# Kernel optimization log

Measured on AMD Instinct MI355X. Metric: run time of the kernel, lower is better.

## Reference

```python
import jax, jax.numpy as jnp
import numpy as np

EPS = 1e-5  # F.instance_norm default eps


def _inorm(x, axis):
    # instance norm (no affine), biased variance, over `axis`
    m = jnp.mean(x, axis=axis, keepdims=True)
    v = jnp.mean((x - m) ** 2, axis=axis, keepdims=True)
    return (x - m) * jax.lax.rsqrt(v + EPS)


def setup_inputs() -> dict:
    key = jax.random.key(0)
    ks = jax.random.split(key, 8)
    C, N, H, W = 256, 8192, 96, 96
    wscale = C ** -0.5  # keep logits in a sane range
    q = jax.random.normal(ks[0], (N, C), jnp.float32)
    k = jax.random.normal(ks[1], (1, C, H, W), jnp.float32)
    qw = jax.random.normal(ks[2], (C, C), jnp.float32) * wscale
    qb = jax.random.normal(ks[3], (C,), jnp.float32) * 0.1
    kw = jax.random.normal(ks[4], (C, C), jnp.float32) * wscale
    kb = jax.random.normal(ks[5], (C,), jnp.float32) * 0.1
    sw = jax.random.normal(ks[6], (C, C), jnp.float32) * wscale
    sb = jax.random.normal(ks[7], (C,), jnp.float32) * 0.1
    return {"q": q, "k": k, "qw": qw, "qb": qb, "kw": kw, "kb": kb, "sw": sw, "sb": sb}


def reference(q, k, qw, qb, kw, kb, sw, sb):
    # q: (N, C) content features; k: (1, C, H, W) style features
    C = q.shape[1]
    qc = q.T                       # (C, N)  == q.T.unsqueeze(0) without batch dim
    st = k[0].reshape(C, -1)       # (C, HW) style values (flattened)

    qn = _inorm(qc, 1)             # instance norm over N per channel
    qe = (qw @ qn + qb[:, None]).T # Conv1d 1x1 -> (N, C)

    kn = _inorm(st, 1)             # instance norm over H*W per channel
    ke = kw @ kn + kb[:, None]     # Conv2d 1x1 -> (C, HW)

    se = (sw @ st + sb[:, None]).T # Conv2d 1x1 -> (HW, C)

    scale = C ** -0.5
    attn = jax.nn.softmax((qe @ ke) * scale, axis=-1)   # (N, HW)

    mean = attn @ se                                    # (N, C)
    var = jax.nn.relu(attn @ (se * se) - mean * mean)   # (N, C)
    std = jnp.sqrt(var)

    cs = qn.T * std + mean          # instance_norm(c) * std + mean, (N, C)
    return cs
```

## Files before the change

kernel.cpp:

```cpp
#include <hip/hip_runtime.h>

typedef __attribute__((ext_vector_type(8))) short short8;
typedef __attribute__((ext_vector_type(4))) float float4v;

#define CDIM 256
#define NQ   8192
#define HWN  9216

static __device__ __forceinline__ unsigned short f2bf(float f) {
  union { float f; unsigned int i; } v; v.f = f;
  unsigned int r = v.i + 0x7FFFu + ((v.i >> 16) & 1u);
  return (unsigned short)(r >> 16);
}

__global__ __launch_bounds__(256) void stats_all_kernel(const float* __restrict__ q, const float* __restrict__ k0,
                                                        float* __restrict__ pq, float* __restrict__ pq2,
                                                        float* __restrict__ mk, float* __restrict__ rk,
                                                        float* __restrict__ sdk) {
  int b = blockIdx.x, t = threadIdx.x;
  if (b < 256) {
    const float4* q4 = (const float4*)(q + (size_t)b * 32 * CDIM);
    float sx = 0, sy = 0, sz = 0, sw = 0, tx = 0, ty = 0, tz = 0, tw = 0;
    for (int i = t; i < 32 * 64; i += 256) {
      float4 v = q4[i];
      sx += v.x; sy += v.y; sz += v.z; sw += v.w;
      tx += v.x * v.x; ty += v.y * v.y; tz += v.z * v.z; tw += v.w * v.w;
    }
    __shared__ float4 sA[256], sB[256];
    sA[t] = make_float4(sx, sy, sz, sw); sB[t] = make_float4(tx, ty, tz, tw);
    __syncthreads();
    if (t < 64) {
      float4 a = sA[t], b2 = sB[t];
      #pragma unroll
      for (int r = 1; r < 4; r++) {
        float4 u = sA[t + r * 64], w2 = sB[t + r * 64];
        a.x += u.x; a.y += u.y; a.z += u.z; a.w += u.w;
        b2.x += w2.x; b2.y += w2.y; b2.z += w2.z; b2.w += w2.w;
      }
      ((float4*)pq)[b * 64 + t] = a;
      ((float4*)pq2)[b * 64 + t] = b2;
    }
  } else {
    __shared__ float rs[256], rs2[256];
    int c = b - 256;
    float s = 0.f, s2 = 0.f;
    const float4* row = (const float4*)(k0 + (size_t)c * HWN);
    for (int j = t; j < HWN / 4; j += 256) {
      float4 v = row[j];
      s += v.x + v.y + v.z + v.w;
      s2 += v.x * v.x + v.y * v.y + v.z * v.z + v.w * v.w;
    }
    rs[t] = s; rs2[t] = s2; __syncthreads();
    for (int off = 128; off > 0; off >>= 1) {
      if (t < off) { rs[t] += rs[t + off]; rs2[t] += rs2[t + off]; }
      __syncthreads();
    }
    if (t == 0) {
      float mean = rs[0] / (float)HWN;
      float var = fmaxf(rs2[0] / (float)HWN - mean * mean, 0.f);
      mk[c] = mean; rk[c] = rsqrtf(var + 1e-5f); sdk[c] = sqrtf(var + 1e-5f);
    }
  }
}

__global__ __launch_bounds__(256) void cvtall_kernel(const float* __restrict__ qw, const float* __restrict__ kw,
                                                     const float* __restrict__ sw, const float* __restrict__ sb,
                                                     unsigned short* __restrict__ qwb, unsigned short* __restrict__ kwb,
                                                     unsigned short* __restrict__ swb2,
                                                     const float* __restrict__ sdk, const float* __restrict__ mk,
                                                     const float* __restrict__ pq, const float* __restrict__ pq2,
                                                     float* __restrict__ mq, float* __restrict__ rq,
                                                     float* __restrict__ bias2) {
  int b = blockIdx.x, t = threadIdx.x;
  if (b < 128) {
    const float* src = b < 64 ? qw : kw;
    unsigned short* dst = b < 64 ? qwb : kwb;
    int i = (b & 63) * 256 + t;
    float4 v = ((const float4*)src)[i];
    union { unsigned short o[4]; uint2 u; } w;
    w.o[0] = f2bf(v.x); w.o[1] = f2bf(v.y); w.o[2] = f2bf(v.z); w.o[3] = f2bf(v.w);
    ((uint2*)dst)[i] = w.u;
  } else if (b < 192) {
    int i = (b - 128) * 256 + t;
    int c0 = (i * 4) & 255;
    float4 v = ((const float4*)sw)[i];
    union { unsigned short o[4]; uint2 u; } w;
    w.o[0] = f2bf(v.x * sdk[c0 + 0]); w.o[1] = f2bf(v.y * sdk[c0 + 1]);
    w.o[2] = f2bf(v.z * sdk[c0 + 2]); w.o[3] = f2bf(v.w * sdk[c0 + 3]);
    ((uint2*)swb2)[i] = w.u;
  } else if (b == 192) {
    int c = t;
    float s = 0, s2 = 0;
    for (int bb = 0; bb < 256; bb++) { s += pq[bb * 256 + c]; s2 += pq2[bb * 256 + c]; }
    float mean = s / (float)NQ;
    float var = s2 / (float)NQ - mean * mean;
    mq[c] = mean; rq[c] = rsqrtf(fmaxf(var, 0.f) + 1e-5f);
  } else {
    int r = t;
    float acc = 0.f;
    for (int k = 0; k < 256; k++) acc += sw[r * 256 + k] * mk[k];
    bias2[r] = acc + sb[r];
  }
}

__global__ __launch_bounds__(256) void ktrans_kernel(const float* __restrict__ k0,
                                                     const float* __restrict__ mk, const float* __restrict__ rk,
                                                     unsigned short* __restrict__ stn) {
  __shared__ float tile[32][33];
  int p0 = blockIdx.x * 32, c0 = blockIdx.y * 32;
  int t = threadIdx.x;
  int pl = t & 31, cl = t >> 5;
  #pragma unroll
  for (int r = 0; r < 4; r++) {
    int c = cl + r * 8;
    tile[c][pl] = k0[(size_t)(c0 + c) * HWN + p0 + pl];
  }
  __syncthreads();
  int cl2 = t & 31, pl2 = t >> 5;
  float mean = mk[c0 + cl2], rinv = rk[c0 + cl2];
  #pragma unroll
  for (int r = 0; r < 4; r++) {
    int p = pl2 + r * 8;
    float f = tile[cl2][p];
    stn[(size_t)(p0 + p) * CDIM + c0 + cl2] = f2bf((f - mean) * rinv);
  }
}

__global__ __launch_bounds__(256) void gemms_kernel(const float* __restrict__ qf,
                                                    const float* __restrict__ mq, const float* __restrict__ rq,
                                                    const unsigned short* __restrict__ qwb, const float* __restrict__ qb,
                                                    unsigned short* __restrict__ Qs,
                                                    const unsigned short* __restrict__ stn,
                                                    const unsigned short* __restrict__ kwb, const float* __restrict__ kb,
                                                    unsigned short* __restrict__ Km,
                                                    const unsigned short* __restrict__ swb2, const float* __restrict__ bias2,
                                                    unsigned short* __restrict__ VseT, unsigned short* __restrict__ Vse2T) {
  int b = blockIdx.x, t = threadIdx.x;
  int w = t >> 6, lane = t & 63, g = lane >> 4, li = lane & 15;
  float4v acc[16];
  #pragma unroll
  for (int i = 0; i < 16; i++) acc[i] = (float4v){0.f, 0.f, 0.f, 0.f};

  if (b < 128) {
    int m0 = b * 64;
    const float* abase = qf + (size_t)(m0 + w * 16 + li) * CDIM + g * 8;
    #pragma unroll
    for (int kc = 0; kc < 8; kc++) {
      int c0 = kc * 32 + g * 8;
      float4 f0 = *(const float4*)(abase + kc * 32);
      float4 f1 = *(const float4*)(abase + kc * 32 + 4);
      float4 m0v = *(const float4*)(mq + c0), m1v = *(const float4*)(mq + c0 + 4);
      float4 r0v = *(const float4*)(rq + c0), r1v = *(const float4*)(rq + c0 + 4);
      union { unsigned short o[8]; short8 s; } a;
      a.o[0] = f2bf((f0.x - m0v.x) * r0v.x); a.o[1] = f2bf((f0.y - m0v.y) * r0v.y);
      a.o[2] = f2bf((f0.z - m0v.z) * r0v.z); a.o[3] = f2bf((f0.w - m0v.w) * r0v.w);
      a.o[4] = f2bf((f1.x - m1v.x) * r1v.x); a.o[5] = f2bf((f1.y - m1v.y) * r1v.y);
      a.o[6] = f2bf((f1.z - m1v.z) * r1v.z); a.o[7] = f2bf((f1.w - m1v.w) * r1v.w);
      #pragma unroll
      for (int ct = 0; ct < 16; ct++) {
        short8 bb = *(const short8*)(qwb + (size_t)(ct * 16 + li) * CDIM + kc * 32 + g * 8);
        acc[ct] = __builtin_amdgcn_mfma_f32_16x16x32_bf16(a.s, bb, acc[ct], 0, 0, 0);
      }
    }
    #pragma unroll
    for (int ct = 0; ct < 16; ct++) {
      int col = ct * 16 + li;
      #pragma unroll
      for (int j = 0; j < 4; j++) {
        int row = m0 + w * 16 + g * 4 + j;
        float v = (acc[ct][j] + qb[col]) * (0.0625f * 1.4426950408889634f);
        Qs[(size_t)row * CDIM + col] = f2bf(v);
      }
    }
  } else if (b < 272) {
    int m0 = (b - 128) * 64;
    const unsigned short* abase = stn + (size_t)(m0 + w * 16 + li) * CDIM + g * 8;
    #pragma unroll
    for (int kc = 0; kc < 8; kc++) {
      short8 a = *(const short8*)(abase + kc * 32);
      #pragma unroll
      for (int ct = 0; ct < 16; ct++) {
        short8 bb = *(const short8*)(kwb + (size_t)(ct * 16 + li) * CDIM + kc * 32 + g * 8);
        acc[ct] = __builtin_amdgcn_mfma_f32_16x16x32_bf16(a, bb, acc[ct], 0, 0, 0);
      }
    }
    #pragma unroll
    for (int ct = 0; ct < 16; ct++) {
      int col = ct * 16 + li;
      #pragma unroll
      for (int j = 0; j < 4; j++) {
        int row = m0 + w * 16 + g * 4 + j;
        Km[(size_t)row * CDIM + col] = f2bf(acc[ct][j] + kb[col]);
      }
    }
  } else {
    int bb2 = b - 272;
    int m0 = (bb2 & 3) * 64, n0 = (bb2 >> 2) * 256;
    const unsigned short* abase = swb2 + (size_t)(m0 + w * 16 + li) * CDIM + g * 8;
    #pragma unroll
    for (int kc = 0; kc < 8; kc++) {
      short8 a = *(const short8*)(abase + kc * 32);
      #pragma unroll
      for (int ct = 0; ct < 16; ct++) {
        short8 bb = *(const short8*)(stn + (size_t)(n0 + ct * 16 + li) * CDIM + kc * 32 + g * 8);
        acc[ct] = __builtin_amdgcn_mfma_f32_16x16x32_bf16(a, bb, acc[ct], 0, 0, 0);
      }
    }
    #pragma unroll
    for (int ct = 0; ct < 16; ct++) {
      int col = n0 + ct * 16 + li;
      #pragma unroll
      for (int j = 0; j < 4; j++) {
        int row = m0 + w * 16 + g * 4 + j;
        float v = acc[ct][j] + bias2[row];
        VseT[(size_t)row * HWN + col] = f2bf(v);
        Vse2T[(size_t)row * HWN + col] = f2bf(v * v);
      }
    }
  }
}

static __device__ __forceinline__ void issue_K(int p0, int w, int lane,
                                               const unsigned short* __restrict__ Km,
                                               unsigned short* K_buf) {
  #pragma unroll
  for (int j2 = 0; j2 < 2; j2++) {
    int i16 = (j2 * 8 + w) * 64 + lane;
    int row = i16 >> 5;
    int chc = (i16 & 31) ^ (row & 15);
    const unsigned short* src = Km + (size_t)(p0 + row) * CDIM + chc * 8;
    unsigned short* dst = K_buf + (j2 * 8 + w) * 512;
    __builtin_amdgcn_global_load_lds((const __attribute__((address_space(1))) unsigned int*)src,
                                     (__attribute__((address_space(3))) unsigned int*)dst, 16, 0, 0);
  }
}

static __device__ __forceinline__ void issue_V(int p0, int w, int lane,
                                               const unsigned short* __restrict__ VseT,
                                               const unsigned short* __restrict__ Vse2T,
                                               unsigned short* V_buf) {
  #pragma unroll
  for (int j2 = 0; j2 < 4; j2++) {
    int i16 = (j2 * 8 + w) * 64 + lane;
    int vd = i16 >> 2;
    int gc = (i16 & 3) ^ ((vd ^ (vd >> 2)) & 3);
    const unsigned short* src = (vd < 256 ? VseT + (size_t)vd * HWN
                                          : Vse2T + (size_t)(vd - 256) * HWN) + p0 + gc * 8;
    unsigned short* dst = V_buf + (j2 * 8 + w) * 512;
    __builtin_amdgcn_global_load_lds((const __attribute__((address_space(1))) unsigned int*)src,
                                     (__attribute__((address_space(3))) unsigned int*)dst, 16, 0, 0);
  }
}

__global__ __launch_bounds__(512, 1) void attn_kernel(const unsigned short* __restrict__ Qs,
                                                      const unsigned short* __restrict__ Km,
                                                      const unsigned short* __restrict__ VseT,
                                                      const unsigned short* __restrict__ Vse2T,
                                                      float* __restrict__ Op, float2* __restrict__ ml,
                                                      int tiles_per_g, int G) {
  __shared__ __align__(16) unsigned short K_lds[2][32 * 256];
  __shared__ __align__(16) unsigned short V_lds[2][512 * 32];
  __shared__ __align__(16) unsigned short P_scr[8 * 640];

  const int t = threadIdx.x;
  const int w = t >> 6, lane = t & 63;
  const int g4 = lane >> 4, li = lane & 15;

  int bid = blockIdx.x, qb, g;
  if (G == 4) { g = (bid & 7) >> 1; qb = ((bid & 1) << 5) + (bid >> 3); }
  else        { g = bid % G;        qb = bid / G; }
  const int n0 = qb * 128;
  const int p_begin = g * tiles_per_g * 32;

  short8 qf[8];
  {
    const unsigned short* qbase = Qs + (size_t)(n0 + w * 16 + li) * CDIM + g4 * 8;
    #pragma unroll
    for (int kc = 0; kc < 8; kc++) qf[kc] = *(const short8*)(qbase + kc * 32);
  }
  float4v O[32];
  #pragma unroll
  for (int i = 0; i < 32; i++) O[i] = (float4v){0.f, 0.f, 0.f, 0.f};
  float4v s_acc = (float4v){0.f, 0.f, 0.f, 0.f};
  float m[4] = {-1e30f, -1e30f, -1e30f, -1e30f};
  const short8 ones = (short8){0x3F80, 0x3F80, 0x3F80, 0x3F80, 0x3F80, 0x3F80, 0x3F80, 0x3F80};

  issue_K(p_begin, w, lane, Km, K_lds[0]);
  issue_V(p_begin, w, lane, VseT, Vse2T, V_lds[0]);

  for (int it = 0; it < tiles_per_g; ++it) {
    asm volatile("s_waitcnt vmcnt(0)" ::: "memory");
    __builtin_amdgcn_s_barrier();
    asm volatile("" ::: "memory");
    if (it + 1 < tiles_per_g) {
      issue_K(p_begin + (it + 1) * 32, w, lane, Km, K_lds[(it + 1) & 1]);
      issue_V(p_begin + (it + 1) * 32, w, lane, VseT, Vse2T, V_lds[(it + 1) & 1]);
    }

    const unsigned short* Kc = K_lds[it & 1];
    float4v S0 = (float4v){0.f, 0.f, 0.f, 0.f}, S1 = (float4v){0.f, 0.f, 0.f, 0.f};
    __builtin_amdgcn_s_setprio(1);
    #pragma unroll
    for (int kc = 0; kc < 8; kc++) {
      int c = kc * 4 + g4;
      short8 b0 = *(const short8*)((const char*)Kc + li * 512 + ((c ^ li) << 4));
      short8 b1 = *(const short8*)((const char*)Kc + (16 + li) * 512 + ((c ^ li) << 4));
      S0 = __builtin_amdgcn_mfma_f32_16x16x32_bf16(qf[kc], b0, S0, 0, 0, 0);
      S1 = __builtin_amdgcn_mfma_f32_16x16x32_bf16(qf[kc], b1, S1, 0, 0, 0);
    }
    __builtin_amdgcn_s_setprio(0);

    float pmax[4], corr[4];
    #pragma unroll
    for (int j = 0; j < 4; j++) {
      float mx = fmaxf(S0[j], S1[j]);
      #pragma unroll
      for (int msk = 1; msk < 16; msk <<= 1) mx = fmaxf(mx, __shfl_xor(mx, msk, 64));
      pmax[j] = mx;
    }
    int needs = ((pmax[0] > m[0] + 5.f) || (pmax[1] > m[1] + 5.f) ||
                 (pmax[2] > m[2] + 5.f) || (pmax[3] > m[3] + 5.f)) ? 1 : 0;
    if (needs) {
      #pragma unroll
      for (int j = 0; j < 4; j++) {
        float mn = fmaxf(m[j], pmax[j]);
        corr[j] = exp2f(m[j] - mn);
        m[j] = mn;
      }
    }
    unsigned short* Pw = P_scr + w * 640;
    #pragma unroll
    for (int j = 0; j < 4; j++) {
      float e0 = exp2f(S0[j] - m[j]);
      float e1 = exp2f(S1[j] - m[j]);
      int row = g4 * 4 + j;
      Pw[row * 40 + li] = f2bf(e0);
      Pw[row * 40 + 16 + li] = f2bf(e1);
    }
    if (__any(needs)) {
      #pragma unroll
      for (int j = 0; j < 4; j++) s_acc[j] *= corr[j];
      #pragma unroll
      for (int i = 0; i < 32; i++) {
        O[i][0] *= corr[0]; O[i][1] *= corr[1]; O[i][2] *= corr[2]; O[i][3] *= corr[3];
      }
    }

    short8 pa = *(const short8*)(Pw + li * 40 + g4 * 8);
    const unsigned short* Vc = V_lds[it & 1];
    __builtin_amdgcn_s_setprio(1);
    s_acc = __builtin_amdgcn_mfma_f32_16x16x32_bf16(pa, ones, s_acc, 0, 0, 0);
    #pragma unroll
    for (int vt = 0; vt < 32; vt++) {
      int vd = vt * 16 + li;
      int kc2 = g4 ^ ((vd ^ (vd >> 2)) & 3);
      short8 vb = *(const short8*)((const char*)Vc + vd * 64 + (kc2 << 4));
      O[vt] = __builtin_amdgcn_mfma_f32_16x16x32_bf16(pa, vb, O[vt], 0, 0, 0);
    }
    __builtin_amdgcn_s_setprio(0);
  }

  #pragma unroll
  for (int vt = 0; vt < 32; vt++) {
    #pragma unroll
    for (int j = 0; j < 4; j++) {
      int n = n0 + w * 16 + g4 * 4 + j;
      int vd = vt * 16 + li;
      Op[((size_t)g * NQ + n) * 512 + vd] = O[vt][j];
    }
  }
  if (li == 0) {
    #pragma unroll
    for (int j = 0; j < 4; j++) {
      int n = n0 + w * 16 + g4 * 4 + j;
      ml[(size_t)g * NQ + n] = make_float2(m[j], s_acc[j]);
    }
  }
}

__global__ __launch_bounds__(256) void combine_kernel(const float* __restrict__ Op, const float2* __restrict__ ml,
                                                      const float* __restrict__ q,
                                                      const float* __restrict__ mq, const float* __restrict__ rq,
                                                      float* __restrict__ out, int G) {
  int t = threadIdx.x;
  int rl = t >> 6, j = t & 63;
  int n = blockIdx.x * 4 + rl, c0 = j * 4;
  __shared__ float wsm[4][8];
  if (j == 0) {
    float mstar = -1e30f;
    float mg[8], lg[8];
    for (int g = 0; g < G; g++) {
      float2 v = ml[(size_t)g * NQ + n];
      mg[g] = v.x; lg[g] = v.y;
      mstar = fmaxf(mstar, v.x);
    }
    float L = 0.f;
    for (int g = 0; g < G; g++) L += lg[g] * exp2f(mg[g] - mstar);
    float Li = 1.f / L;
    for (int g = 0; g < G; g++) wsm[rl][g] = exp2f(mg[g] - mstar) * Li;
  }
  __syncthreads();
  float4 of = make_float4(0, 0, 0, 0), o2 = make_float4(0, 0, 0, 0);
  for (int g = 0; g < G; g++) {
    size_t base = ((size_t)g * NQ + n) * 512;
    float wg = wsm[rl][g];
    float4 a = *(const float4*)(Op + base + c0);
    float4 b = *(const float4*)(Op + base + 256 + c0);
    of.x += wg * a.x; of.y += wg * a.y; of.z += wg * a.z; of.w += wg * a.w;
    o2.x += wg * b.x; o2.y += wg * b.y; o2.z += wg * b.z; o2.w += wg * b.w;
  }
  float4 qv = *(const float4*)(q + (size_t)n * CDIM + c0);
  float4 mv = *(const float4*)(mq + c0);
  float4 rv = *(const float4*)(rq + c0);
  float4 ov;
  ov.x = (qv.x - mv.x) * rv.x * sqrtf(fmaxf(o2.x - of.x * of.x, 0.f)) + of.x;
  ov.y = (qv.y - mv.y) * rv.y * sqrtf(fmaxf(o2.y - of.y * of.y, 0.f)) + of.y;
  ov.z = (qv.z - mv.z) * rv.z * sqrtf(fmaxf(o2.z - of.z * of.z, 0.f)) + of.z;
  ov.w = (qv.w - mv.w) * rv.w * sqrtf(fmaxf(o2.w - of.w * of.w, 0.f)) + of.w;
  *(float4*)(out + (size_t)n * CDIM + c0) = ov;
}

extern "C" void kernel_launch(void* const* d_in, const int* in_sizes, int n_in,
                              void* d_out, int out_size, void* d_ws, size_t ws_size,
                              hipStream_t stream) {
  const float* q  = (const float*)d_in[0];
  const float* k0 = (const float*)d_in[1];
  const float* qw = (const float*)d_in[2];
  const float* qb = (const float*)d_in[3];
  const float* kw = (const float*)d_in[4];
  const float* kb = (const float*)d_in[5];
  const float* sw = (const float*)d_in[6];
  const float* sb = (const float*)d_in[7];
  float* out = (float*)d_out;

  char* ws = (char*)d_ws;
  float* mq   = (float*)ws; ws += 1024;
  float* rq   = (float*)ws; ws += 1024;
  float* mk   = (float*)ws; ws += 1024;
  float* rk   = (float*)ws; ws += 1024;
  float* sdk  = (float*)ws; ws += 1024;
  float* bias2= (float*)ws; ws += 1024;
  float* pq   = (float*)ws; ws += 256 * 256 * 4;
  float* pq2  = (float*)ws; ws += 256 * 256 * 4;
  unsigned short* qwb  = (unsigned short*)ws; ws += 65536 * 2;
  unsigned short* kwb  = (unsigned short*)ws; ws += 65536 * 2;
  unsigned short* swb2 = (unsigned short*)ws; ws += 65536 * 2;
  unsigned short* Qs    = (unsigned short*)ws; ws += (size_t)NQ * CDIM * 2;
  unsigned short* stn   = (unsigned short*)ws; ws += (size_t)HWN * CDIM * 2;
  unsigned short* Km    = (unsigned short*)ws; ws += (size_t)HWN * CDIM * 2;
  unsigned short* VseT  = (unsigned short*)ws; ws += (size_t)HWN * CDIM * 2;
  unsigned short* Vse2T = (unsigned short*)ws; ws += (size_t)HWN * CDIM * 2;

  size_t base_used = (size_t)(ws - (char*)d_ws);
  int G = 4;
  const int gcand[3] = {4, 2, 1};
  for (int i = 0; i < 3; i++) {
    G = gcand[i];
    size_t need = base_used + (size_t)G * ((size_t)NQ * 512 * 4 + (size_t)NQ * 8);
    if (need <= ws_size) break;
  }
  float*  Opart = (float*)ws;                 ws += (size_t)G * NQ * 512 * 4;
  float2* mlp   = (float2*)ws;                ws += (size_t)G * NQ * 8;
  int tiles_per_g = (HWN / 32) / G;

  stats_all_kernel<<<512, 256, 0, stream>>>(q, k0, pq, pq2, mk, rk, sdk);
  cvtall_kernel<<<194, 256, 0, stream>>>(qw, kw, sw, sb, qwb, kwb, swb2, sdk, mk, pq, pq2, mq, rq, bias2);
  ktrans_kernel<<<dim3(HWN / 32, CDIM / 32), 256, 0, stream>>>(k0, mk, rk, stn);
  gemms_kernel<<<416, 256, 0, stream>>>(q, mq, rq, qwb, qb, Qs, stn, kwb, kb, Km, swb2, bias2, VseT, Vse2T);
  attn_kernel<<<dim3(64 * G), 512, 0, stream>>>(Qs, Km, VseT, Vse2T, Opart, mlp, tiles_per_g, G);
  combine_kernel<<<NQ / 4, 256, 0, stream>>>(Opart, mlp, q, mq, rq, out, G);
}
```

Baseline: 304.4 us.

## Software-pipeline attention PV with shared P tiles and triple-buffered V

Restructures the attention loop so each wave computes PV for a 64-column slice of V across all 128 query rows, using P tiles shared through LDS. The PV step of the previous tile runs after the current QK step, and V is triple-buffered so the next loads are issued before the wait. Rescale factors now pass between waves through LDS, and the lazy-rescale threshold moves from 5 to 8. The style-value path also changes: it now uses the raw, un-normalized style features in bf16 with the plain bias, instead of normalized features multiplied by a stored std. This adds an extra buffer written by ktrans at the end of the workspace. The extra barriers per tile, more LDS use and the larger threshold carry a small precision risk.

```diff
diff --git a/kernel.cpp b/kernel.cpp
--- a/kernel.cpp
+++ b/kernel.cpp
@@ -15,8 +15,7 @@
 
 __global__ __launch_bounds__(256) void stats_all_kernel(const float* __restrict__ q, const float* __restrict__ k0,
                                                         float* __restrict__ pq, float* __restrict__ pq2,
-                                                        float* __restrict__ mk, float* __restrict__ rk,
-                                                        float* __restrict__ sdk) {
+                                                        float* __restrict__ mk, float* __restrict__ rk) {
   int b = blockIdx.x, t = threadIdx.x;
   if (b < 256) {
     const float4* q4 = (const float4*)(q + (size_t)b * 32 * CDIM);
@@ -58,54 +57,39 @@
     if (t == 0) {
       float mean = rs[0] / (float)HWN;
       float var = fmaxf(rs2[0] / (float)HWN - mean * mean, 0.f);
-      mk[c] = mean; rk[c] = rsqrtf(var + 1e-5f); sdk[c] = sqrtf(var + 1e-5f);
+      mk[c] = mean; rk[c] = rsqrtf(var + 1e-5f);
     }
   }
 }
 
 __global__ __launch_bounds__(256) void cvtall_kernel(const float* __restrict__ qw, const float* __restrict__ kw,
-                                                     const float* __restrict__ sw, const float* __restrict__ sb,
+                                                     const float* __restrict__ sw,
                                                      unsigned short* __restrict__ qwb, unsigned short* __restrict__ kwb,
-                                                     unsigned short* __restrict__ swb2,
-                                                     const float* __restrict__ sdk, const float* __restrict__ mk,
+                                                     unsigned short* __restrict__ swb,
                                                      const float* __restrict__ pq, const float* __restrict__ pq2,
-                                                     float* __restrict__ mq, float* __restrict__ rq,
-                                                     float* __restrict__ bias2) {
+                                                     float* __restrict__ mq, float* __restrict__ rq) {
   int b = blockIdx.x, t = threadIdx.x;
-  if (b < 128) {
-    const float* src = b < 64 ? qw : kw;
-    unsigned short* dst = b < 64 ? qwb : kwb;
+  if (b < 192) {
+    const float* src = b < 64 ? qw : (b < 128 ? kw : sw);
+    unsigned short* dst = b < 64 ? qwb : (b < 128 ? kwb : swb);
     int i = (b & 63) * 256 + t;
     float4 v = ((const float4*)src)[i];
     union { unsigned short o[4]; uint2 u; } w;
     w.o[0] = f2bf(v.x); w.o[1] = f2bf(v.y); w.o[2] = f2bf(v.z); w.o[3] = f2bf(v.w);
     ((uint2*)dst)[i] = w.u;
-  } else if (b < 192) {
-    int i = (b - 128) * 256 + t;
-    int c0 = (i * 4) & 255;
-    float4 v = ((const float4*)sw)[i];
-    union { unsigned short o[4]; uint2 u; } w;
-    w.o[0] = f2bf(v.x * sdk[c0 + 0]); w.o[1] = f2bf(v.y * sdk[c0 + 1]);
-    w.o[2] = f2bf(v.z * sdk[c0 + 2]); w.o[3] = f2bf(v.w * sdk[c0 + 3]);
-    ((uint2*)swb2)[i] = w.u;
-  } else if (b == 192) {
+  } else {
     int c = t;
     float s = 0, s2 = 0;
     for (int bb = 0; bb < 256; bb++) { s += pq[bb * 256 + c]; s2 += pq2[bb * 256 + c]; }
     float mean = s / (float)NQ;
     float var = s2 / (float)NQ - mean * mean;
     mq[c] = mean; rq[c] = rsqrtf(fmaxf(var, 0.f) + 1e-5f);
-  } else {
-    int r = t;
-    float acc = 0.f;
-    for (int k = 0; k < 256; k++) acc += sw[r * 256 + k] * mk[k];
-    bias2[r] = acc + sb[r];
   }
 }
 
 __global__ __launch_bounds__(256) void ktrans_kernel(const float* __restrict__ k0,
                                                      const float* __restrict__ mk, const float* __restrict__ rk,
-                                                     unsigned short* __restrict__ stn) {
+                                                     unsigned short* __restrict__ stT, unsigned short* __restrict__ stn) {
   __shared__ float tile[32][33];
   int p0 = blockIdx.x * 32, c0 = blockIdx.y * 32;
   int t = threadIdx.x;
@@ -122,6 +106,7 @@
   for (int r = 0; r < 4; r++) {
     int p = pl2 + r * 8;
     float f = tile[cl2][p];
+    stT[(size_t)(p0 + p) * CDIM + c0 + cl2] = f2bf(f);
     stn[(size_t)(p0 + p) * CDIM + c0 + cl2] = f2bf((f - mean) * rinv);
   }
 }
@@ -133,7 +118,8 @@
                                                     const unsigned short* __restrict__ stn,
                                                     const unsigned short* __restrict__ kwb, const float* __restrict__ kb,
                                                     unsigned short* __restrict__ Km,
-                                                    const unsigned short* __restrict__ swb2, const float* __restrict__ bias2,
+                                                    const unsigned short* __restrict__ swb, const float* __restrict__ sbf,
+                                                    const unsigned short* __restrict__ stT,
                                                     unsigned short* __restrict__ VseT, unsigned short* __restrict__ Vse2T) {
   int b = blockIdx.x, t = threadIdx.x;
   int w = t >> 6, lane = t & 63, g = lane >> 4, li = lane & 15;
@@ -196,13 +182,13 @@
   } else {
     int bb2 = b - 272;
     int m0 = (bb2 & 3) * 64, n0 = (bb2 >> 2) * 256;
-    const unsigned short* abase = swb2 + (size_t)(m0 + w * 16 + li) * CDIM + g * 8;
+    const unsigned short* abase = swb + (size_t)(m0 + w * 16 + li) * CDIM + g * 8;
     #pragma unroll
     for (int kc = 0; kc < 8; kc++) {
       short8 a = *(const short8*)(abase + kc * 32);
       #pragma unroll
       for (int ct = 0; ct < 16; ct++) {
-        short8 bb = *(const short8*)(stn + (size_t)(n0 + ct * 16 + li) * CDIM + kc * 32 + g * 8);
+        short8 bb = *(const short8*)(stT + (size_t)(n0 + ct * 16 + li) * CDIM + kc * 32 + g * 8);
         acc[ct] = __builtin_amdgcn_mfma_f32_16x16x32_bf16(a, bb, acc[ct], 0, 0, 0);
       }
     }
@@ -212,7 +198,7 @@
       #pragma unroll
       for (int j = 0; j < 4; j++) {
         int row = m0 + w * 16 + g * 4 + j;
-        float v = acc[ct][j] + bias2[row];
+        float v = acc[ct][j] + sbf[row];
         VseT[(size_t)row * HWN + col] = f2bf(v);
         Vse2T[(size_t)row * HWN + col] = f2bf(v * v);
       }
@@ -242,10 +228,10 @@
   #pragma unroll
   for (int j2 = 0; j2 < 4; j2++) {
     int i16 = (j2 * 8 + w) * 64 + lane;
-    int vd = i16 >> 2;
-    int gc = (i16 & 3) ^ ((vd ^ (vd >> 2)) & 3);
-    const unsigned short* src = (vd < 256 ? VseT + (size_t)vd * HWN
-                                          : Vse2T + (size_t)(vd - 256) * HWN) + p0 + gc * 8;
+    int vrow = i16 >> 2;
+    int chunk = (i16 & 3) ^ ((vrow >> 1) & 3);
+    const unsigned short* src = (vrow < 256 ? VseT + (size_t)vrow * HWN
+                                            : Vse2T + (size_t)(vrow - 256) * HWN) + p0 + chunk * 8;
     unsigned short* dst = V_buf + (j2 * 8 + w) * 512;
     __builtin_amdgcn_global_load_lds((const __attribute__((address_space(1))) unsigned int*)src,
                                      (__attribute__((address_space(3))) unsigned int*)dst, 16, 0, 0);
@@ -259,8 +245,10 @@
                                                       float* __restrict__ Op, float2* __restrict__ ml,
                                                       int tiles_per_g, int G) {
   __shared__ __align__(16) unsigned short K_lds[2][32 * 256];
-  __shared__ __align__(16) unsigned short V_lds[2][512 * 32];
-  __shared__ __align__(16) unsigned short P_scr[8 * 640];
+  __shared__ __align__(16) unsigned short V_lds[3][512 * 32];
+  __shared__ __align__(16) unsigned short P_lds[2][128 * 40];
+  __shared__ float corr_lds[128];
+  __shared__ int needflag[8];
 
   const int t = threadIdx.x;
   const int w = t >> 6, lane = t & 63;
@@ -278,24 +266,48 @@
     #pragma unroll
     for (int kc = 0; kc < 8; kc++) qf[kc] = *(const short8*)(qbase + kc * 32);
   }
-  float4v O[32];
-  #pragma unroll
-  for (int i = 0; i < 32; i++) O[i] = (float4v){0.f, 0.f, 0.f, 0.f};
+  float4v O[8][4];
+  #pragma unroll
+  for (int r = 0; r < 8; r++)
+    #pragma unroll
+    for (int v = 0; v < 4; v++) O[r][v] = (float4v){0.f, 0.f, 0.f, 0.f};
   float4v s_acc = (float4v){0.f, 0.f, 0.f, 0.f};
   float m[4] = {-1e30f, -1e30f, -1e30f, -1e30f};
   const short8 ones = (short8){0x3F80, 0x3F80, 0x3F80, 0x3F80, 0x3F80, 0x3F80, 0x3F80, 0x3F80};
 
+#define PV_BLOCK(P_buf, V_buf)                                                               \
+  {                                                                                          \
+    short8 vb[4];                                                                            \
+    _Pragma("unroll")                                                                        \
+    for (int v = 0; v < 4; v++) {                                                            \
+      int vrow = w * 64 + v * 16 + li;                                                       \
+      vb[v] = *(const short8*)((const char*)(V_buf) + vrow * 64 + ((g4 ^ ((vrow >> 1) & 3)) << 4)); \
+    }                                                                                        \
+    __builtin_amdgcn_s_setprio(1);                                                           \
+    _Pragma("unroll")                                                                        \
+    for (int r = 0; r < 8; r++) {                                                            \
+      short8 pa = *(const short8*)((P_buf) + (r * 16 + li) * 40 + g4 * 8);                   \
+      if (r == w) s_acc = __builtin_amdgcn_mfma_f32_16x16x32_bf16(pa, ones, s_acc, 0, 0, 0); \
+      _Pragma("unroll")                                                                      \
+      for (int v = 0; v < 4; v++)                                                            \
+        O[r][v] = __builtin_amdgcn_mfma_f32_16x16x32_bf16(pa, vb[v], O[r][v], 0, 0, 0);      \
+    }                                                                                        \
+    __builtin_amdgcn_s_setprio(0);                                                           \
+  }
+
   issue_K(p_begin, w, lane, Km, K_lds[0]);
   issue_V(p_begin, w, lane, VseT, Vse2T, V_lds[0]);
 
   for (int it = 0; it < tiles_per_g; ++it) {
-    asm volatile("s_waitcnt vmcnt(0)" ::: "memory");
+    if (it + 1 < tiles_per_g) {
+      issue_K(p_begin + (it + 1) * 32, w, lane, Km, K_lds[(it + 1) & 1]);
+      issue_V(p_begin + (it + 1) * 32, w, lane, VseT, Vse2T, V_lds[(it + 1) % 3]);
+      asm volatile("s_waitcnt vmcnt(6)" ::: "memory");
+    } else {
+      asm volatile("s_waitcnt vmcnt(0)" ::: "memory");
+    }
     __builtin_amdgcn_s_barrier();
     asm volatile("" ::: "memory");
-    if (it + 1 < tiles_per_g) {
-      issue_K(p_begin + (it + 1) * 32, w, lane, Km, K_lds[(it + 1) & 1]);
-      issue_V(p_begin + (it + 1) * 32, w, lane, VseT, Vse2T, V_lds[(it + 1) & 1]);
-    }
 
     const unsigned short* Kc = K_lds[it & 1];
     float4v S0 = (float4v){0.f, 0.f, 0.f, 0.f}, S1 = (float4v){0.f, 0.f, 0.f, 0.f};
@@ -310,6 +322,8 @@
     }
     __builtin_amdgcn_s_setprio(0);
 
+    if (it > 0) PV_BLOCK(P_lds[(it - 1) & 1], V_lds[(it - 1) % 3]);
+
     float pmax[4], corr[4];
     #pragma unroll
     for (int j = 0; j < 4; j++) {
@@ -318,8 +332,8 @@
       for (int msk = 1; msk < 16; msk <<= 1) mx = fmaxf(mx, __shfl_xor(mx, msk, 64));
       pmax[j] = mx;
     }
-    int needs = ((pmax[0] > m[0] + 5.f) || (pmax[1] > m[1] + 5.f) ||
-                 (pmax[2] > m[2] + 5.f) || (pmax[3] > m[3] + 5.f)) ? 1 : 0;
+    int needs = ((pmax[0] > m[0] + 8.f) || (pmax[1] > m[1] + 8.f) ||
+                 (pmax[2] > m[2] + 8.f) || (pmax[3] > m[3] + 8.f)) ? 1 : 0;
     if (needs) {
       #pragma unroll
       for (int j = 0; j < 4; j++) {
@@ -327,46 +341,60 @@
         corr[j] = exp2f(m[j] - mn);
         m[j] = mn;
       }
-    }
-    unsigned short* Pw = P_scr + w * 640;
+    } else {
+      corr[0] = corr[1] = corr[2] = corr[3] = 1.f;
+    }
+    int wany = __any(needs) ? 1 : 0;
+    unsigned short* Pw = P_lds[it & 1];
     #pragma unroll
     for (int j = 0; j < 4; j++) {
       float e0 = exp2f(S0[j] - m[j]);
       float e1 = exp2f(S1[j] - m[j]);
-      int row = g4 * 4 + j;
+      int row = w * 16 + g4 * 4 + j;
       Pw[row * 40 + li] = f2bf(e0);
       Pw[row * 40 + 16 + li] = f2bf(e1);
-    }
-    if (__any(needs)) {
+      if (li == 0) corr_lds[row] = corr[j];
+    }
+    if (lane == 0) needflag[w] = wany;
+
+    asm volatile("s_waitcnt lgkmcnt(0)" ::: "memory");
+    __builtin_amdgcn_s_barrier();
+    asm volatile("" ::: "memory");
+
+    int any = __any(needflag[lane & 7] != 0);
+    if (any) {
       #pragma unroll
       for (int j = 0; j < 4; j++) s_acc[j] *= corr[j];
       #pragma unroll
-      for (int i = 0; i < 32; i++) {
-        O[i][0] *= corr[0]; O[i][1] *= corr[1]; O[i][2] *= corr[2]; O[i][3] *= corr[3];
-      }
-    }
-
-    short8 pa = *(const short8*)(Pw + li * 40 + g4 * 8);
-    const unsigned short* Vc = V_lds[it & 1];
-    __builtin_amdgcn_s_setprio(1);
-    s_acc = __builtin_amdgcn_mfma_f32_16x16x32_bf16(pa, ones, s_acc, 0, 0, 0);
-    #pragma unroll
-    for (int vt = 0; vt < 32; vt++) {
-      int vd = vt * 16 + li;
-      int kc2 = g4 ^ ((vd ^ (vd >> 2)) & 3);
-      short8 vb = *(const short8*)((const char*)Vc + vd * 64 + (kc2 << 4));
-      O[vt] = __builtin_amdgcn_mfma_f32_16x16x32_bf16(pa, vb, O[vt], 0, 0, 0);
-    }
-    __builtin_amdgcn_s_setprio(0);
-  }
-
-  #pragma unroll
-  for (int vt = 0; vt < 32; vt++) {
-    #pragma unroll
-    for (int j = 0; j < 4; j++) {
-      int n = n0 + w * 16 + g4 * 4 + j;
-      int vd = vt * 16 + li;
-      Op[((size_t)g * NQ + n) * 512 + vd] = O[vt][j];
+      for (int r = 0; r < 8; r++) {
+        float c0 = corr_lds[r * 16 + g4 * 4 + 0];
+        float c1 = corr_lds[r * 16 + g4 * 4 + 1];
+        float c2 = corr_lds[r * 16 + g4 * 4 + 2];
+        float c3 = corr_lds[r * 16 + g4 * 4 + 3];
+        #pragma unroll
+        for (int v = 0; v < 4; v++) {
+          O[r][v][0] *= c0; O[r][v][1] *= c1; O[r][v][2] *= c2; O[r][v][3] *= c3;
+        }
+      }
+    }
+  }
+
+  {
+    int tl = tiles_per_g - 1;
+    PV_BLOCK(P_lds[tl & 1], V_lds[tl % 3]);
+  }
+#undef PV_BLOCK
+
+  #pragma unroll
+  for (int r = 0; r < 8; r++) {
+    #pragma unroll
+    for (int v = 0; v < 4; v++) {
+      #pragma unroll
+      for (int j = 0; j < 4; j++) {
+        int n = n0 + r * 16 + g4 * 4 + j;
+        int vd = w * 64 + v * 16 + li;
+        Op[((size_t)g * NQ + n) * 512 + vd] = O[r][v][j];
+      }
     }
   }
   if (li == 0) {
@@ -438,18 +466,19 @@
   float* rq   = (float*)ws; ws += 1024;
   float* mk   = (float*)ws; ws += 1024;
   float* rk   = (float*)ws; ws += 1024;
-  float* sdk  = (float*)ws; ws += 1024;
-  float* bias2= (float*)ws; ws += 1024;
   float* pq   = (float*)ws; ws += 256 * 256 * 4;
   float* pq2  = (float*)ws; ws += 256 * 256 * 4;
-  unsigned short* qwb  = (unsigned short*)ws; ws += 65536 * 2;
-  unsigned short* kwb  = (unsigned short*)ws; ws += 65536 * 2;
-  unsigned short* swb2 = (unsigned short*)ws; ws += 65536 * 2;
+  unsigned short* qwb = (unsigned short*)ws; ws += 65536 * 2;
+  unsigned short* kwb = (unsigned short*)ws; ws += 65536 * 2;
+  unsigned short* swb = (unsigned short*)ws; ws += 65536 * 2;
   unsigned short* Qs    = (unsigned short*)ws; ws += (size_t)NQ * CDIM * 2;
   unsigned short* stn   = (unsigned short*)ws; ws += (size_t)HWN * CDIM * 2;
   unsigned short* Km    = (unsigned short*)ws; ws += (size_t)HWN * CDIM * 2;
   unsigned short* VseT  = (unsigned short*)ws; ws += (size_t)HWN * CDIM * 2;
   unsigned short* Vse2T = (unsigned short*)ws; ws += (size_t)HWN * CDIM * 2;
+
+  unsigned short* stT = (unsigned short*)((char*)d_ws +
+                          ((ws_size - (size_t)HWN * CDIM * 2) & ~(size_t)15));
 
   size_t base_used = (size_t)(ws - (char*)d_ws);
   int G = 4;
@@ -463,10 +492,10 @@
   float2* mlp   = (float2*)ws;                ws += (size_t)G * NQ * 8;
   int tiles_per_g = (HWN / 32) / G;
 
-  stats_all_kernel<<<512, 256, 0, stream>>>(q, k0, pq, pq2, mk, rk, sdk);
-  cvtall_kernel<<<194, 256, 0, stream>>>(qw, kw, sw, sb, qwb, kwb, swb2, sdk, mk, pq, pq2, mq, rq, bias2);
-  ktrans_kernel<<<dim3(HWN / 32, CDIM / 32), 256, 0, stream>>>(k0, mk, rk, stn);
-  gemms_kernel<<<416, 256, 0, stream>>>(q, mq, rq, qwb, qb, Qs, stn, kwb, kb, Km, swb2, bias2, VseT, Vse2T);
+  stats_all_kernel<<<512, 256, 0, stream>>>(q, k0, pq, pq2, mk, rk);
+  cvtall_kernel<<<193, 256, 0, stream>>>(qw, kw, sw, qwb, kwb, swb, pq, pq2, mq, rq);
+  ktrans_kernel<<<dim3(HWN / 32, CDIM / 32), 256, 0, stream>>>(k0, mk, rk, stT, stn);
+  gemms_kernel<<<416, 256, 0, stream>>>(q, mq, rq, qwb, qb, Qs, stn, kwb, kb, Km, swb, sb, stT, VseT, Vse2T);
   attn_kernel<<<dim3(64 * G), 512, 0, stream>>>(Qs, Km, VseT, Vse2T, Opart, mlp, tiles_per_g, G);
   combine_kernel<<<NQ / 4, 256, 0, stream>>>(Opart, mlp, q, mq, rq, out, G);
 }
```

After: 287.0 us. 5.7% less time.
